# Kernel optimization log

Measured on AMD Instinct MI355X. Metric: run time of the kernel, lower is better.

The kernel has to match this reference:

```python
import jax, jax.numpy as jnp
import numpy as np

B, T, D, H = 64, 1024, 256, 256

def setup_inputs() -> dict:
    key = jax.random.key(0)
    k1, k2, k3 = jax.random.split(key, 3)
    s = 1.0 / np.sqrt(H)
    return {
        "x": jax.random.normal(k1, (B, T, D), dtype=jnp.float32),
        "W_ih": jax.random.uniform(k2, (H, D), dtype=jnp.float32, minval=-s, maxval=s),
        "W_hh": jax.random.uniform(k3, (H, H), dtype=jnp.float32, minval=-s, maxval=s),
        "b_ih": jnp.zeros((H,), dtype=jnp.float32),
        "b_hh": jnp.zeros((H,), dtype=jnp.float32),
    }

def reference(x, W_ih, W_hh, b_ih, b_hh):
    # Precompute input projections for all timesteps at once (same math,
    # avoids T small GEMMs): [B, T, H]
    x_proj = jnp.einsum("btd,hd->bth", x, W_ih) + b_ih
    h0 = jnp.zeros((x.shape[0], W_hh.shape[0]), dtype=x.dtype)

    def step(h, xp_t):
        h_new = jnp.tanh(xp_t + h @ W_hh.T + b_hh)
        return h_new, h_new  # output of vanilla RNN cell is the new hidden state

    # scan over time: xp time-major [T, B, H]
    _, outs = jax.lax.scan(step, h0, jnp.swapaxes(x_proj, 0, 1))
    return jnp.swapaxes(outs, 0, 1)  # [B, T, H]
```

## Files before the change

kernel.cpp:

```cpp
#include <hip/hip_runtime.h>

#define BB 64
#define TT 1024
#define DD 256
#define HH 256

typedef float vf4 __attribute__((ext_vector_type(4)));
typedef float vf2 __attribute__((ext_vector_type(2)));
struct alignas(16) v2x2 { vf2 lo, hi; };

#define LD4(p) (*(const vf4*)(p))
#define LDW(p) (*(const v2x2*)(p))

__device__ __forceinline__ float fast_tanh(float x) {
    float e = __expf(2.0f * x);
    return 1.0f - 2.0f / (e + 1.0f);
}

#define PKFMA(acc, aa, bb) acc = __builtin_elementwise_fma((aa), (bb), (acc))

#define DPPADD(dst, src, CTRL) {                                                   \
    int _di = __builtin_amdgcn_update_dpp(0, __float_as_int(src), CTRL, 0xF, 0xF, true); \
    dst = (src) + __int_as_float(_di); }

#define FMR(rr, bb, ss)                   \
    rr.x = fmaf((ss), (bb).x, rr.x);      \
    rr.y = fmaf((ss), (bb).y, rr.y);      \
    rr.z = fmaf((ss), (bb).z, rr.z);      \
    rr.w = fmaf((ss), (bb).w, rr.w)

#define BKb 32
#define LDP 132

__global__ __attribute__((amdgpu_flat_work_group_size(256, 256),
                          amdgpu_waves_per_eu(4, 4)))
void xproj_kernel(const float* __restrict__ x, const float* __restrict__ W_ih,
                  const float* __restrict__ b_ih, float* __restrict__ xp)
{
    __shared__ float As[BKb][LDP];
    __shared__ float Bs[BKb][LDP];

    const int tid = threadIdx.x;
    const int nb = blockIdx.x & 1;
    const int mb = blockIdx.x >> 1;
    const int m0 = mb * 128;
    const int n0 = nb * 128;

    const int sr = tid >> 3;
    const int sk = (tid & 7) * 4;

    const int tx = tid & 15;
    const int ty = tid >> 4;
    const int ma = ty * 4, mh = 64 + ty * 4;
    const int na = tx * 4, nh = 64 + tx * 4;

    vf4 ra0 = 0, ra1 = 0, ra2 = 0, ra3 = 0, ra4 = 0, ra5 = 0, ra6 = 0, ra7 = 0;
    vf4 rb0 = 0, rb1 = 0, rb2 = 0, rb3 = 0, rb4 = 0, rb5 = 0, rb6 = 0, rb7 = 0;

    for (int k0 = 0; k0 < DD; k0 += BKb) {
        #pragma unroll
        for (int g = 0; g < 4; ++g) {
            const int r = sr + g * 32;
            const vf4 v = LD4(x + (size_t)(m0 + r) * DD + k0 + sk);
            As[sk + 0][r] = v.x; As[sk + 1][r] = v.y;
            As[sk + 2][r] = v.z; As[sk + 3][r] = v.w;
        }
        #pragma unroll
        for (int g = 0; g < 4; ++g) {
            const int n = sr + g * 32;
            const vf4 v = LD4(W_ih + (size_t)(n0 + n) * DD + k0 + sk);
            Bs[sk + 0][n] = v.x; Bs[sk + 1][n] = v.y;
            Bs[sk + 2][n] = v.z; Bs[sk + 3][n] = v.w;
        }
        __syncthreads();

        #pragma unroll
        for (int kk = 0; kk < BKb; ++kk) {
            const vf4 alo = LD4(&As[kk][ma]);
            const vf4 ahi = LD4(&As[kk][mh]);
            const vf4 bl  = LD4(&Bs[kk][na]);
            const vf4 bh  = LD4(&Bs[kk][nh]);
            FMR(ra0, bl, alo.x); FMR(rb0, bh, alo.x);
            FMR(ra1, bl, alo.y); FMR(rb1, bh, alo.y);
            FMR(ra2, bl, alo.z); FMR(rb2, bh, alo.z);
            FMR(ra3, bl, alo.w); FMR(rb3, bh, alo.w);
            FMR(ra4, bl, ahi.x); FMR(rb4, bh, ahi.x);
            FMR(ra5, bl, ahi.y); FMR(rb5, bh, ahi.y);
            FMR(ra6, bl, ahi.z); FMR(rb6, bh, ahi.z);
            FMR(ra7, bl, ahi.w); FMR(rb7, bh, ahi.w);
        }
        __syncthreads();
    }

    const vf4 bia = LD4(b_ih + n0 + na);
    const vf4 bib = LD4(b_ih + n0 + nh);

    #define STORE_ROW(m, rA, rB)                                   \
        {                                                          \
            float* outp = xp + (size_t)(m0 + (m)) * HH + n0;       \
            *(vf4*)(outp + na) = rA + bia;                         \
            *(vf4*)(outp + nh) = rB + bib;                         \
        }
    STORE_ROW(ma + 0, ra0, rb0); STORE_ROW(ma + 1, ra1, rb1);
    STORE_ROW(ma + 2, ra2, rb2); STORE_ROW(ma + 3, ra3, rb3);
    STORE_ROW(mh + 0, ra4, rb4); STORE_ROW(mh + 1, ra5, rb5);
    STORE_ROW(mh + 2, ra6, rb6); STORE_ROW(mh + 3, ra7, rb7);
    #undef STORE_ROW
}

__global__ __attribute__((amdgpu_flat_work_group_size(1024, 1024),
                          amdgpu_waves_per_eu(4, 4)))
void rnn_kernel(const float* __restrict__ W_hh, const float* __restrict__ b_hh,
                const float* __restrict__ xpin, float* __restrict__ hout)
{
    const int tid = threadIdx.x;
    const int jg = tid >> 4;
    const int c  = tid & 15;
    const int j0 = jg * 4;
    const int jmine = j0 + (c & 3);
    const int b = blockIdx.x;

    __shared__ float hbuf[2][16 * 20];

    const float* wr0 = W_hh + (size_t)(j0 + 0) * HH + c * 16;
    const float* wr1 = W_hh + (size_t)(j0 + 1) * HH + c * 16;
    const float* wr2 = W_hh + (size_t)(j0 + 2) * HH + c * 16;
    const float* wr3 = W_hh + (size_t)(j0 + 3) * HH + c * 16;
    v2x2 w00 = LDW(wr0 + 0), w01 = LDW(wr0 + 4), w02 = LDW(wr0 + 8), w03 = LDW(wr0 + 12);
    v2x2 w10 = LDW(wr1 + 0), w11 = LDW(wr1 + 4), w12 = LDW(wr1 + 8), w13 = LDW(wr1 + 12);
    v2x2 w20 = LDW(wr2 + 0), w21 = LDW(wr2 + 4), w22 = LDW(wr2 + 8), w23 = LDW(wr2 + 12);
    v2x2 w30 = LDW(wr3 + 0), w31 = LDW(wr3 + 4), w32 = LDW(wr3 + 8), w33 = LDW(wr3 + 12);
    const float bias = b_hh[jmine];

    if (tid < 320) hbuf[0][tid] = 0.0f;
    __syncthreads();

    const float* pj = xpin + (size_t)b * TT * HH + jmine;
    float*       po = hout + (size_t)b * TT * HH + jmine;
    const int haddr = ((jmine >> 4) * 20) + (jmine & 15);

    float xp0 = pj[0];
    float xp1 = pj[HH];

    int p = 0;
    for (int t = 0; t < TT; ++t) {
        asm volatile("" : "+v"(w00.lo), "+v"(w00.hi), "+v"(w01.lo), "+v"(w01.hi),
                          "+v"(w02.lo), "+v"(w02.hi), "+v"(w03.lo), "+v"(w03.hi),
                          "+v"(w10.lo), "+v"(w10.hi), "+v"(w11.lo), "+v"(w11.hi),
                          "+v"(w12.lo), "+v"(w12.hi), "+v"(w13.lo), "+v"(w13.hi));
        asm volatile("" : "+v"(w20.lo), "+v"(w20.hi), "+v"(w21.lo), "+v"(w21.hi),
                          "+v"(w22.lo), "+v"(w22.hi), "+v"(w23.lo), "+v"(w23.hi),
                          "+v"(w30.lo), "+v"(w30.hi), "+v"(w31.lo), "+v"(w31.hi),
                          "+v"(w32.lo), "+v"(w32.hi), "+v"(w33.lo), "+v"(w33.hi));

        const int tn = (t + 2 < TT) ? (t + 2) : (TT - 1);
        const float xpn = pj[(size_t)tn * HH];

        const float* hc = &hbuf[p][c * 20];
        const v2x2 h0 = LDW(hc + 0), h1 = LDW(hc + 4),
                   h2 = LDW(hc + 8), h3 = LDW(hc + 12);

        vf2 a0 = {0.f, 0.f}, a1 = {0.f, 0.f}, a2 = {0.f, 0.f}, a3 = {0.f, 0.f};
        PKFMA(a0, w00.lo, h0.lo); PKFMA(a1, w10.lo, h0.lo);
        PKFMA(a2, w20.lo, h0.lo); PKFMA(a3, w30.lo, h0.lo);
        PKFMA(a0, w00.hi, h0.hi); PKFMA(a1, w10.hi, h0.hi);
        PKFMA(a2, w20.hi, h0.hi); PKFMA(a3, w30.hi, h0.hi);
        PKFMA(a0, w01.lo, h1.lo); PKFMA(a1, w11.lo, h1.lo);
        PKFMA(a2, w21.lo, h1.lo); PKFMA(a3, w31.lo, h1.lo);
        PKFMA(a0, w01.hi, h1.hi); PKFMA(a1, w11.hi, h1.hi);
        PKFMA(a2, w21.hi, h1.hi); PKFMA(a3, w31.hi, h1.hi);
        PKFMA(a0, w02.lo, h2.lo); PKFMA(a1, w12.lo, h2.lo);
        PKFMA(a2, w22.lo, h2.lo); PKFMA(a3, w32.lo, h2.lo);
        PKFMA(a0, w02.hi, h2.hi); PKFMA(a1, w12.hi, h2.hi);
        PKFMA(a2, w22.hi, h2.hi); PKFMA(a3, w32.hi, h2.hi);
        PKFMA(a0, w03.lo, h3.lo); PKFMA(a1, w13.lo, h3.lo);
        PKFMA(a2, w23.lo, h3.lo); PKFMA(a3, w33.lo, h3.lo);
        PKFMA(a0, w03.hi, h3.hi); PKFMA(a1, w13.hi, h3.hi);
        PKFMA(a2, w23.hi, h3.hi); PKFMA(a3, w33.hi, h3.hi);

        const float s0 = a0.x + a0.y, s1 = a1.x + a1.y,
                    s2 = a2.x + a2.y, s3 = a3.x + a3.y;

        float t0, t1, t2, t3, b0v, b1v, u0, u1, vfin;
        DPPADD(t0, s0, 0xB1); DPPADD(t1, s1, 0xB1);
        DPPADD(t2, s2, 0xB1); DPPADD(t3, s3, 0xB1);
        b0v = (c & 1) ? t1 : t0;
        b1v = (c & 1) ? t3 : t2;
        DPPADD(u0, b0v, 0x4E); DPPADD(u1, b1v, 0x4E);
        vfin = (c & 2) ? u1 : u0;
        DPPADD(vfin, vfin, 0x124);
        DPPADD(vfin, vfin, 0x128);

        const float hn = fast_tanh(vfin + xp0 + bias);
        if (c < 4) {
            hbuf[1 - p][haddr] = hn;
            po[(size_t)t * HH] = hn;
        }
        xp0 = xp1;
        xp1 = xpn;
        p ^= 1;
        __syncthreads();
    }
}

extern "C" void kernel_launch(void* const* d_in, const int* in_sizes, int n_in,
                              void* d_out, int out_size, void* d_ws, size_t ws_size,
                              hipStream_t stream) {
    const float* x    = (const float*)d_in[0];
    const float* W_ih = (const float*)d_in[1];
    const float* W_hh = (const float*)d_in[2];
    const float* b_ih = (const float*)d_in[3];
    const float* b_hh = (const float*)d_in[4];
    float* out = (float*)d_out;

    const size_t xp_bytes = (size_t)BB * TT * HH * sizeof(float);
    float* xp = (ws_size >= xp_bytes) ? (float*)d_ws : out;

    xproj_kernel<<<dim3(512 * 2), dim3(256), 0, stream>>>(x, W_ih, b_ih, xp);
    rnn_kernel<<<dim3(BB), dim3(1024), 0, stream>>>(W_hh, b_hh, xp, out);
}
```

Baseline: 916.6 us.

## Stage xproj inputs and hidden outputs through LDS in 8-step chunks

The recurrent kernel now loads precomputed input projections for 8 timesteps at a time into double-buffered shared memory, using coalesced vf2 loads prefetched two chunks ahead. Outputs are collected in a shared buffer and written back as one coalesced chunk per 8 steps. Previously each step issued scattered per-element global loads and stores from only a quarter of the lanes. This cuts global memory transactions on the serial critical path, at the cost of about 32KB of extra LDS and an extra shared-memory store inside the last step of each chunk.

```diff
diff --git a/kernel.cpp b/kernel.cpp
--- a/kernel.cpp
+++ b/kernel.cpp
@@ -4,12 +4,15 @@
 #define TT 1024
 #define DD 256
 #define HH 256
+#define CH 8
+#define NCH (TT / CH)
 
 typedef float vf4 __attribute__((ext_vector_type(4)));
 typedef float vf2 __attribute__((ext_vector_type(2)));
 struct alignas(16) v2x2 { vf2 lo, hi; };
 
 #define LD4(p) (*(const vf4*)(p))
+#define LD2(p) (*(const vf2*)(p))
 #define LDW(p) (*(const v2x2*)(p))
 
 __device__ __forceinline__ float fast_tanh(float x) {
@@ -121,6 +124,8 @@
     const int b = blockIdx.x;
 
     __shared__ float hbuf[2][16 * 20];
+    __shared__ float xchk[2][CH * HH];
+    __shared__ float obuf[2][CH * HH];
 
     const float* wr0 = W_hh + (size_t)(j0 + 0) * HH + c * 16;
     const float* wr1 = W_hh + (size_t)(j0 + 1) * HH + c * 16;
@@ -132,74 +137,84 @@
     v2x2 w30 = LDW(wr3 + 0), w31 = LDW(wr3 + 4), w32 = LDW(wr3 + 8), w33 = LDW(wr3 + 12);
     const float bias = b_hh[jmine];
 
+    const float* xbase = xpin + (size_t)b * TT * HH;
+    float*       obase = hout + (size_t)b * TT * HH;
+    const int haddr = ((jmine >> 4) * 20) + (jmine & 15);
+
+    vf2 r = LD2(xbase + tid * 2);
     if (tid < 320) hbuf[0][tid] = 0.0f;
+    *(vf2*)&xchk[0][tid * 2] = r;
+    r = LD2(xbase + CH * HH + tid * 2);
     __syncthreads();
 
-    const float* pj = xpin + (size_t)b * TT * HH + jmine;
-    float*       po = hout + (size_t)b * TT * HH + jmine;
-    const int haddr = ((jmine >> 4) * 20) + (jmine & 15);
-
-    float xp0 = pj[0];
-    float xp1 = pj[HH];
-
-    int p = 0;
-    for (int t = 0; t < TT; ++t) {
-        asm volatile("" : "+v"(w00.lo), "+v"(w00.hi), "+v"(w01.lo), "+v"(w01.hi),
-                          "+v"(w02.lo), "+v"(w02.hi), "+v"(w03.lo), "+v"(w03.hi),
-                          "+v"(w10.lo), "+v"(w10.hi), "+v"(w11.lo), "+v"(w11.hi),
-                          "+v"(w12.lo), "+v"(w12.hi), "+v"(w13.lo), "+v"(w13.hi));
-        asm volatile("" : "+v"(w20.lo), "+v"(w20.hi), "+v"(w21.lo), "+v"(w21.hi),
-                          "+v"(w22.lo), "+v"(w22.hi), "+v"(w23.lo), "+v"(w23.hi),
-                          "+v"(w30.lo), "+v"(w30.hi), "+v"(w31.lo), "+v"(w31.hi),
-                          "+v"(w32.lo), "+v"(w32.hi), "+v"(w33.lo), "+v"(w33.hi));
-
-        const int tn = (t + 2 < TT) ? (t + 2) : (TT - 1);
-        const float xpn = pj[(size_t)tn * HH];
-
-        const float* hc = &hbuf[p][c * 20];
-        const v2x2 h0 = LDW(hc + 0), h1 = LDW(hc + 4),
-                   h2 = LDW(hc + 8), h3 = LDW(hc + 12);
-
-        vf2 a0 = {0.f, 0.f}, a1 = {0.f, 0.f}, a2 = {0.f, 0.f}, a3 = {0.f, 0.f};
-        PKFMA(a0, w00.lo, h0.lo); PKFMA(a1, w10.lo, h0.lo);
-        PKFMA(a2, w20.lo, h0.lo); PKFMA(a3, w30.lo, h0.lo);
-        PKFMA(a0, w00.hi, h0.hi); PKFMA(a1, w10.hi, h0.hi);
-        PKFMA(a2, w20.hi, h0.hi); PKFMA(a3, w30.hi, h0.hi);
-        PKFMA(a0, w01.lo, h1.lo); PKFMA(a1, w11.lo, h1.lo);
-        PKFMA(a2, w21.lo, h1.lo); PKFMA(a3, w31.lo, h1.lo);
-        PKFMA(a0, w01.hi, h1.hi); PKFMA(a1, w11.hi, h1.hi);
-        PKFMA(a2, w21.hi, h1.hi); PKFMA(a3, w31.hi, h1.hi);
-        PKFMA(a0, w02.lo, h2.lo); PKFMA(a1, w12.lo, h2.lo);
-        PKFMA(a2, w22.lo, h2.lo); PKFMA(a3, w32.lo, h2.lo);
-        PKFMA(a0, w02.hi, h2.hi); PKFMA(a1, w12.hi, h2.hi);
-        PKFMA(a2, w22.hi, h2.hi); PKFMA(a3, w32.hi, h2.hi);
-        PKFMA(a0, w03.lo, h3.lo); PKFMA(a1, w13.lo, h3.lo);
-        PKFMA(a2, w23.lo, h3.lo); PKFMA(a3, w33.lo, h3.lo);
-        PKFMA(a0, w03.hi, h3.hi); PKFMA(a1, w13.hi, h3.hi);
-        PKFMA(a2, w23.hi, h3.hi); PKFMA(a3, w33.hi, h3.hi);
-
-        const float s0 = a0.x + a0.y, s1 = a1.x + a1.y,
-                    s2 = a2.x + a2.y, s3 = a3.x + a3.y;
-
-        float t0, t1, t2, t3, b0v, b1v, u0, u1, vfin;
-        DPPADD(t0, s0, 0xB1); DPPADD(t1, s1, 0xB1);
-        DPPADD(t2, s2, 0xB1); DPPADD(t3, s3, 0xB1);
-        b0v = (c & 1) ? t1 : t0;
-        b1v = (c & 1) ? t3 : t2;
-        DPPADD(u0, b0v, 0x4E); DPPADD(u1, b1v, 0x4E);
-        vfin = (c & 2) ? u1 : u0;
-        DPPADD(vfin, vfin, 0x124);
-        DPPADD(vfin, vfin, 0x128);
-
-        const float hn = fast_tanh(vfin + xp0 + bias);
-        if (c < 4) {
-            hbuf[1 - p][haddr] = hn;
-            po[(size_t)t * HH] = hn;
-        }
-        xp0 = xp1;
-        xp1 = xpn;
-        p ^= 1;
-        __syncthreads();
+    for (int ci = 0; ci < NCH; ++ci) {
+        const int cb = ci & 1;
+
+        #pragma unroll
+        for (int s = 0; s < CH; ++s) {
+            asm volatile("" : "+v"(w00.lo), "+v"(w00.hi), "+v"(w01.lo), "+v"(w01.hi),
+                              "+v"(w02.lo), "+v"(w02.hi), "+v"(w03.lo), "+v"(w03.hi),
+                              "+v"(w10.lo), "+v"(w10.hi), "+v"(w11.lo), "+v"(w11.hi),
+                              "+v"(w12.lo), "+v"(w12.hi), "+v"(w13.lo), "+v"(w13.hi));
+            asm volatile("" : "+v"(w20.lo), "+v"(w20.hi), "+v"(w21.lo), "+v"(w21.hi),
+                              "+v"(w22.lo), "+v"(w22.hi), "+v"(w23.lo), "+v"(w23.hi),
+                              "+v"(w30.lo), "+v"(w30.hi), "+v"(w31.lo), "+v"(w31.hi),
+                              "+v"(w32.lo), "+v"(w32.hi), "+v"(w33.lo), "+v"(w33.hi));
+
+            const float xpv = xchk[cb][s * HH + jmine];
+
+            const float* hc = &hbuf[s & 1][c * 20];
+            const v2x2 h0 = LDW(hc + 0), h1 = LDW(hc + 4),
+                       h2 = LDW(hc + 8), h3 = LDW(hc + 12);
+
+            vf2 a0 = {0.f, 0.f}, a1 = {0.f, 0.f}, a2 = {0.f, 0.f}, a3 = {0.f, 0.f};
+            PKFMA(a0, w00.lo, h0.lo); PKFMA(a1, w10.lo, h0.lo);
+            PKFMA(a2, w20.lo, h0.lo); PKFMA(a3, w30.lo, h0.lo);
+            PKFMA(a0, w00.hi, h0.hi); PKFMA(a1, w10.hi, h0.hi);
+            PKFMA(a2, w20.hi, h0.hi); PKFMA(a3, w30.hi, h0.hi);
+            PKFMA(a0, w01.lo, h1.lo); PKFMA(a1, w11.lo, h1.lo);
+            PKFMA(a2, w21.lo, h1.lo); PKFMA(a3, w31.lo, h1.lo);
+            PKFMA(a0, w01.hi, h1.hi); PKFMA(a1, w11.hi, h1.hi);
+            PKFMA(a2, w21.hi, h1.hi); PKFMA(a3, w31.hi, h1.hi);
+            PKFMA(a0, w02.lo, h2.lo); PKFMA(a1, w12.lo, h2.lo);
+            PKFMA(a2, w22.lo, h2.lo); PKFMA(a3, w32.lo, h2.lo);
+            PKFMA(a0, w02.hi, h2.hi); PKFMA(a1, w12.hi, h2.hi);
+            PKFMA(a2, w22.hi, h2.hi); PKFMA(a3, w32.hi, h2.hi);
+            PKFMA(a0, w03.lo, h3.lo); PKFMA(a1, w13.lo, h3.lo);
+            PKFMA(a2, w23.lo, h3.lo); PKFMA(a3, w33.lo, h3.lo);
+            PKFMA(a0, w03.hi, h3.hi); PKFMA(a1, w13.hi, h3.hi);
+            PKFMA(a2, w23.hi, h3.hi); PKFMA(a3, w33.hi, h3.hi);
+
+            const float s0 = a0.x + a0.y, s1 = a1.x + a1.y,
+                        s2 = a2.x + a2.y, s3 = a3.x + a3.y;
+
+            float t0, t1, t2, t3, b0v, b1v, u0, u1, vfin;
+            DPPADD(t0, s0, 0xB1); DPPADD(t1, s1, 0xB1);
+            DPPADD(t2, s2, 0xB1); DPPADD(t3, s3, 0xB1);
+            b0v = (c & 1) ? t1 : t0;
+            b1v = (c & 1) ? t3 : t2;
+            DPPADD(u0, b0v, 0x4E); DPPADD(u1, b1v, 0x4E);
+            vfin = (c & 2) ? u1 : u0;
+            DPPADD(vfin, vfin, 0x124);
+            DPPADD(vfin, vfin, 0x128);
+
+            if (s == CH - 1 && ci != NCH - 1) {
+                *(vf2*)&xchk[cb ^ 1][tid * 2] = r;
+            }
+
+            const float hn = fast_tanh(vfin + xpv + bias);
+            if (c < 4) {
+                hbuf[1 - (s & 1)][haddr] = hn;
+                obuf[cb][s * HH + jmine] = hn;
+            }
+            __syncthreads();
+        }
+
+        const vf2 ov = *(const vf2*)&obuf[cb][tid * 2];
+        *(vf2*)(obase + (size_t)ci * CH * HH + tid * 2) = ov;
+        if (ci + 2 < NCH) {
+            r = LD2(xbase + (size_t)(ci + 2) * CH * HH + tid * 2);
+        }
     }
 }
 
```

New measurement: 855.3 us. 6.7% less time.
